# Kernel optimization log

Measured on AMD Instinct MI355X. Metric: run time of the kernel, lower is better.

## Reference

```python
import jax, jax.numpy as jnp
import numpy as np

B = 4096
D = 256
TEMP = 0.5


def setup_inputs() -> dict:
    key = jax.random.key(0)
    k1, k2 = jax.random.split(key)
    x_i = jax.random.normal(k1, (B, D), dtype=jnp.float32)
    x_j = jax.random.normal(k2, (B, D), dtype=jnp.float32)
    return {"x_i": x_i, "x_j": x_j}


def reference(x_i, x_j):
    b = x_i.shape[0]
    # L2-normalize rows (F.normalize with default eps=1e-12)
    def l2norm(x):
        n = jnp.linalg.norm(x, axis=1, keepdims=True)
        return x / jnp.maximum(n, 1e-12)

    z = jnp.concatenate([l2norm(x_i), l2norm(x_j)], axis=0)  # [2B, D]
    # rows of z are unit-norm, so cosine similarity == dot product
    sim = z @ z.T  # [2B, 2B]

    # positives: diagonals at offsets +B and -B
    idx = jnp.arange(b)
    sim_ij = sim[idx, idx + b]
    sim_ji = sim[idx + b, idx]
    pos = jnp.concatenate([sim_ij, sim_ji], axis=0)  # [2B]

    nom = jnp.exp(pos / TEMP)
    neg_mask = 1.0 - jnp.eye(2 * b, dtype=sim.dtype)
    denom = jnp.sum(neg_mask * jnp.exp(sim / TEMP), axis=1)  # [2B]
    loss = jnp.sum(-jnp.log(nom / denom)) / (2 * b)
    return loss
```

## Files before the change

kernel.cpp:

```cpp
#include <hip/hip_runtime.h>

#define NB   4096
#define ND   256
#define N2B  8192
#define INV_T 2.0f
#define NBAND 64
#define NTRI  2080

typedef __attribute__((ext_vector_type(8))) short bf16x8;
typedef __attribute__((ext_vector_type(4))) float f32x4;

__device__ __forceinline__ void gload_lds16(const void* g, void* l) {
  __builtin_amdgcn_global_load_lds(
      (const __attribute__((address_space(1))) void*)g,
      (__attribute__((address_space(3))) void*)l, 16, 0, 0);
}

__device__ __forceinline__ unsigned short f2b(float f) {
  unsigned int u = __float_as_uint(f);
  u = (u + 0x7fffu + ((u >> 16) & 1u)) >> 16;
  return (unsigned short)u;
}
__device__ __forceinline__ float b2f(unsigned short h) {
  return __uint_as_float(((unsigned int)h) << 16);
}

__global__ __launch_bounds__(256) void k_normalize(
    const float* __restrict__ xi, const float* __restrict__ xj,
    unsigned short* __restrict__ Z, float* __restrict__ diagE,
    float* __restrict__ pos, float* __restrict__ lossAcc,
    unsigned int* __restrict__ ticket) {
  __shared__ float sh[2][256];
  if (blockIdx.x == 0 && threadIdx.x == 0) { *lossAcc = 0.0f; *ticket = 0u; }
  int wave = threadIdx.x >> 6, lane = threadIdx.x & 63;
  int r = (int)blockIdx.x * 2 + (wave & 1);
  bool isJ = wave >= 2;
  const float* src = (isJ ? xj : xi) + (size_t)r * ND;
  int zrow = r + (isJ ? NB : 0);

  float4 v = *(const float4*)(src + lane * 4);
  float ss = v.x * v.x + v.y * v.y + v.z * v.z + v.w * v.w;
#pragma unroll
  for (int m = 1; m < 64; m <<= 1) ss += __shfl_xor(ss, m, 64);
  float scale = 1.0f / fmaxf(sqrtf(ss), 1e-12f);
  unsigned short h0 = f2b(v.x * scale), h1 = f2b(v.y * scale);
  unsigned short h2 = f2b(v.z * scale), h3 = f2b(v.w * scale);
  ushort4 st; st.x = h0; st.y = h1; st.z = h2; st.w = h3;
  *(ushort4*)(Z + (size_t)zrow * ND + lane * 4) = st;

  float f0 = b2f(h0), f1 = b2f(h1), f2 = b2f(h2), f3 = b2f(h3);
  float d = f0 * f0 + f1 * f1 + f2 * f2 + f3 * f3;
#pragma unroll
  for (int m = 1; m < 64; m <<= 1) d += __shfl_xor(d, m, 64);
  if (lane == 0) diagE[zrow] = __expf(d * INV_T);

  if (isJ) {
    float* s = sh[wave & 1] + lane * 4;
    s[0] = f0; s[1] = f1; s[2] = f2; s[3] = f3;
  }
  __syncthreads();
  if (!isJ) {
    const float* s = sh[wave] + lane * 4;
    float p = f0 * s[0] + f1 * s[1] + f2 * s[2] + f3 * s[3];
#pragma unroll
    for (int m = 1; m < 64; m <<= 1) p += __shfl_xor(p, m, 64);
    if (lane == 0) pos[r] = p;
  }
}

__global__ __launch_bounds__(512, 4) void k_sym(
    const unsigned short* __restrict__ Z, float* __restrict__ P) {
  __shared__ alignas(16) unsigned short Bs[128 * ND];

  int tid = threadIdx.x;
  int wave = tid >> 6, lane = tid & 63;
  int quad = lane >> 4, c16 = lane & 15;

  int g = ((int)blockIdx.x & 7) * (NTRI / 8) + ((int)blockIdx.x >> 3);
  int SI = 0, SJ = 0, u = g;
  bool found = false;
  for (int si = 0; si < 8 && !found; ++si) {
    for (int sj = si; sj < 8; ++sj) {
      int sz = (si == sj) ? 36 : 64;
      if (u < sz) { SI = si; SJ = sj; found = true; break; }
      u -= sz;
    }
  }
  int ti, tj;
  if (SI == SJ) {
    ti = 0;
    while (u >= 8 - ti) { u -= 8 - ti; ++ti; }
    tj = ti + u;
  } else {
    ti = u >> 3; tj = u & 7;
  }
  int I = SI * 8 + ti, J = SJ * 8 + tj;
  bool diag = (I == J);

  int rowA = I * 128, rowB = J * 128;

  int lr1 = lane >> 5, cs = lane & 31;
#pragma unroll
  for (int j = 0; j < 8; ++j) {
    int r0 = wave * 16 + j * 2;
    int row = r0 + lr1;
    int gc = cs ^ (row & 31);
    gload_lds16(Z + (size_t)(rowB + row) * ND + gc * 8, &Bs[r0 * ND]);
  }

  bf16x8 afr[8];
  int wrow = rowA + wave * 16;
#pragma unroll
  for (int kk = 0; kk < 8; ++kk)
    afr[kk] = *(const bf16x8*)(Z + (size_t)(wrow + c16) * ND + kk * 32 +
                               quad * 8);

  asm volatile("s_waitcnt vmcnt(0)" ::: "memory");
  __syncthreads();

  f32x4 acc[8] = {};
  __builtin_amdgcn_s_setprio(1);
#pragma unroll
  for (int kk = 0; kk < 8; ++kk) {
    bf16x8 bfr[8];
#pragma unroll
    for (int ni = 0; ni < 8; ++ni) {
      int row = ni * 16 + c16;
      int slot = (kk * 4 + quad) ^ (row & 31);
      bfr[ni] = *(const bf16x8*)&Bs[row * ND + slot * 8];
    }
#pragma unroll
    for (int ni = 0; ni < 8; ++ni)
      acc[ni] = __builtin_amdgcn_mfma_f32_16x16x32_bf16(afr[kk], bfr[ni],
                                                        acc[ni], 0, 0, 0);
  }
  __builtin_amdgcn_s_setprio(0);

  float rs[4] = {0.0f, 0.0f, 0.0f, 0.0f};
  float csum[8];
#pragma unroll
  for (int ni = 0; ni < 8; ++ni) csum[ni] = 0.0f;

#pragma unroll
  for (int ni = 0; ni < 8; ++ni)
#pragma unroll
    for (int r = 0; r < 4; ++r) {
      float e = __expf(acc[ni][r] * INV_T);
      rs[r] += e;
      csum[ni] += e;
    }

#pragma unroll
  for (int m = 1; m <= 8; m <<= 1)
#pragma unroll
    for (int r = 0; r < 4; ++r) rs[r] += __shfl_xor(rs[r], m, 64);

#pragma unroll
  for (int r = 0; r < 4; ++r)
    if (c16 == r) {
      int row = wrow + quad * 4 + r;
      P[(size_t)row * NBAND + J] = rs[r];
    }

  if (!diag) {
#pragma unroll
    for (int ni = 0; ni < 8; ++ni) {
      csum[ni] += __shfl_xor(csum[ni], 16, 64);
      csum[ni] += __shfl_xor(csum[ni], 32, 64);
    }
    __syncthreads();
    float* colred = (float*)Bs;
    if (lane < 16) {
#pragma unroll
      for (int ni = 0; ni < 8; ++ni)
        colred[wave * 128 + ni * 16 + lane] = csum[ni];
    }
    __syncthreads();
    if (tid < 128) {
      float v = 0.0f;
#pragma unroll
      for (int w = 0; w < 8; ++w) v += colred[w * 128 + tid];
      P[(size_t)(rowB + tid) * NBAND + I] = v;
    }
  }
}

__global__ __launch_bounds__(256) void k_final(
    const float* __restrict__ P, const float* __restrict__ diagE,
    const float* __restrict__ pos, float* __restrict__ lossAcc,
    unsigned int* __restrict__ ticket, float* __restrict__ out) {
  __shared__ float red[4];
  int tid = threadIdx.x;
  int wave = tid >> 6, lane = tid & 63;
  int row = (int)blockIdx.x * 256 + tid;

  const float4* Pr = (const float4*)(P + (size_t)row * NBAND);
  float s = 0.0f;
#pragma unroll
  for (int q = 0; q < 16; ++q) {
    float4 a = Pr[q];
    s += (a.x + a.y) + (a.z + a.w);
  }
  s -= diagE[row];
  float term = __logf(s) - INV_T * pos[row & (NB - 1)];
#pragma unroll
  for (int m = 1; m < 64; m <<= 1) term += __shfl_xor(term, m, 64);
  if (lane == 0) red[wave] = term;
  __syncthreads();
  if (tid == 0) {
    float bs = red[0] + red[1] + red[2] + red[3];
    atomicAdd(lossAcc, bs);
    __threadfence();
    unsigned int old = atomicAdd(ticket, 1u);
    if (old == 31u) {
      float v = atomicAdd(lossAcc, 0.0f);
      out[0] = v * (1.0f / (float)N2B);
    }
  }
}

extern "C" void kernel_launch(void* const* d_in, const int* in_sizes, int n_in,
                              void* d_out, int out_size, void* d_ws,
                              size_t ws_size, hipStream_t stream) {
  const float* xi = (const float*)d_in[0];
  const float* xj = (const float*)d_in[1];
  float* out = (float*)d_out;
  char* ws = (char*)d_ws;
  unsigned short* Z = (unsigned short*)ws;
  float* P = (float*)(ws + (4u << 20));
  float* pos = (float*)(ws + (6u << 20));
  float* diagE = (float*)(ws + (6u << 20) + 65536);
  float* lossAcc = (float*)(ws + (6u << 20) + 131072);
  unsigned int* ticket = (unsigned int*)(ws + (6u << 20) + 131072 + 64);

  k_normalize<<<dim3(NB / 2), dim3(256), 0, stream>>>(xi, xj, Z, diagE, pos,
                                                      lossAcc, ticket);
  k_sym<<<dim3(NTRI), dim3(512), 0, stream>>>(Z, P);
  k_final<<<dim3(32), dim3(256), 0, stream>>>(P, diagE, pos, lossAcc, ticket,
                                              out);
}
```

Measured before the change: 109.0 us.

## Make k_sym persistent over row strips with double-buffered LDS tiles

Each block now keeps one 128-row A strip resident in registers and walks up to four 128-column B blocks in 64-row half tiles. The next half tile is prefetched into a second LDS buffer while the current one runs through MFMA, and the launch shrinks from 2080 triangular tiles to 544 blocks. The goal is to amortise A loads and block launch and index-decode cost, and to overlap global-to-LDS transfers with compute. In exchange each block has more serial iterations with a barrier per step, fewer blocks are in flight, and some blocks do less work than others, which can leave compute units idle.

```diff
diff --git a/kernel.cpp b/kernel.cpp
--- a/kernel.cpp
+++ b/kernel.cpp
@@ -5,7 +5,7 @@
 #define N2B  8192
 #define INV_T 2.0f
 #define NBAND 64
-#define NTRI  2080
+#define NBLK  544
 
 typedef __attribute__((ext_vector_type(8))) short bf16x8;
 typedef __attribute__((ext_vector_type(4))) float f32x4;
@@ -70,117 +70,128 @@
 
 __global__ __launch_bounds__(512, 4) void k_sym(
     const unsigned short* __restrict__ Z, float* __restrict__ P) {
-  __shared__ alignas(16) unsigned short Bs[128 * ND];
+  __shared__ alignas(16) unsigned short ldsU[32768];
+  __shared__ float colred[2][8][64];
 
   int tid = threadIdx.x;
   int wave = tid >> 6, lane = tid & 63;
   int quad = lane >> 4, c16 = lane & 15;
-
-  int g = ((int)blockIdx.x & 7) * (NTRI / 8) + ((int)blockIdx.x >> 3);
-  int SI = 0, SJ = 0, u = g;
-  bool found = false;
-  for (int si = 0; si < 8 && !found; ++si) {
-    for (int sj = si; sj < 8; ++sj) {
-      int sz = (si == sj) ? 36 : 64;
-      if (u < sz) { SI = si; SJ = sj; found = true; break; }
-      u -= sz;
-    }
-  }
-  int ti, tj;
-  if (SI == SJ) {
-    ti = 0;
-    while (u >= 8 - ti) { u -= 8 - ti; ++ti; }
-    tj = ti + u;
-  } else {
-    ti = u >> 3; tj = u & 7;
-  }
-  int I = SI * 8 + ti, J = SJ * 8 + tj;
-  bool diag = (I == J);
-
-  int rowA = I * 128, rowB = J * 128;
-
   int lr1 = lane >> 5, cs = lane & 31;
+
+  int g = ((int)blockIdx.x & 7) * (NBLK / 8) + ((int)blockIdx.x >> 3);
+  int I = 0, acc0 = 0;
+  while (acc0 + ((64 - I + 3) >> 2) <= g) { acc0 += (64 - I + 3) >> 2; ++I; }
+  int k = g - acc0;
+  int b0 = I + 4 * k;
+  int nb = min(4, 64 - b0);
+  int nt = nb * 2;
+  int q0 = b0 * 2;
+  int rowA = I * 128;
+
 #pragma unroll
   for (int j = 0; j < 8; ++j) {
     int r0 = wave * 16 + j * 2;
     int row = r0 + lr1;
     int gc = cs ^ (row & 31);
-    gload_lds16(Z + (size_t)(rowB + row) * ND + gc * 8, &Bs[r0 * ND]);
-  }
+    gload_lds16(Z + (size_t)(rowA + row) * ND + gc * 8, &ldsU[r0 * ND]);
+  }
+  asm volatile("s_waitcnt vmcnt(0)" ::: "memory");
+  __syncthreads();
 
   bf16x8 afr[8];
+  {
+    int arow = wave * 16 + c16;
+    const unsigned short* ap = &ldsU[arow * ND];
+    int ax = arow & 31;
+#pragma unroll
+    for (int kk = 0; kk < 8; ++kk)
+      afr[kk] = *(const bf16x8*)&ap[((kk * 4 + quad) ^ ax) * 8];
+  }
+  asm volatile("s_waitcnt lgkmcnt(0)" ::: "memory");
+  __syncthreads();
+
+  auto STAGE = [&](int t, int h) {
+    int base = (q0 + t) * 64;
+#pragma unroll
+    for (int j = 0; j < 4; ++j) {
+      int r0 = wave * 8 + j * 2;
+      int row = r0 + lr1;
+      int gc = cs ^ (row & 31);
+      gload_lds16(Z + (size_t)(base + row) * ND + gc * 8,
+                  &ldsU[h * 16384 + r0 * ND]);
+    }
+  };
+
+  STAGE(0, 0);
+  asm volatile("s_waitcnt vmcnt(0)" ::: "memory");
+  __syncthreads();
+
   int wrow = rowA + wave * 16;
-#pragma unroll
-  for (int kk = 0; kk < 8; ++kk)
-    afr[kk] = *(const bf16x8*)(Z + (size_t)(wrow + c16) * ND + kk * 32 +
-                               quad * 8);
-
-  asm volatile("s_waitcnt vmcnt(0)" ::: "memory");
-  __syncthreads();
-
-  f32x4 acc[8] = {};
-  __builtin_amdgcn_s_setprio(1);
-#pragma unroll
-  for (int kk = 0; kk < 8; ++kk) {
-    bf16x8 bfr[8];
-#pragma unroll
-    for (int ni = 0; ni < 8; ++ni) {
-      int row = ni * 16 + c16;
-      int slot = (kk * 4 + quad) ^ (row & 31);
-      bfr[ni] = *(const bf16x8*)&Bs[row * ND + slot * 8];
-    }
-#pragma unroll
-    for (int ni = 0; ni < 8; ++ni)
-      acc[ni] = __builtin_amdgcn_mfma_f32_16x16x32_bf16(afr[kk], bfr[ni],
-                                                        acc[ni], 0, 0, 0);
-  }
-  __builtin_amdgcn_s_setprio(0);
-
   float rs[4] = {0.0f, 0.0f, 0.0f, 0.0f};
-  float csum[8];
-#pragma unroll
-  for (int ni = 0; ni < 8; ++ni) csum[ni] = 0.0f;
-
-#pragma unroll
-  for (int ni = 0; ni < 8; ++ni)
-#pragma unroll
-    for (int r = 0; r < 4; ++r) {
-      float e = __expf(acc[ni][r] * INV_T);
-      rs[r] += e;
-      csum[ni] += e;
-    }
-
-#pragma unroll
-  for (int m = 1; m <= 8; m <<= 1)
-#pragma unroll
-    for (int r = 0; r < 4; ++r) rs[r] += __shfl_xor(rs[r], m, 64);
-
-#pragma unroll
-  for (int r = 0; r < 4; ++r)
-    if (c16 == r) {
-      int row = wrow + quad * 4 + r;
-      P[(size_t)row * NBAND + J] = rs[r];
-    }
-
-  if (!diag) {
-#pragma unroll
-    for (int ni = 0; ni < 8; ++ni) {
-      csum[ni] += __shfl_xor(csum[ni], 16, 64);
-      csum[ni] += __shfl_xor(csum[ni], 32, 64);
-    }
+
+  for (int t = 0; t < nt; ++t) {
+    int h = t & 1;
+    if (t + 1 < nt) STAGE(t + 1, h ^ 1);
+
+    f32x4 acc[4] = {};
+    __builtin_amdgcn_s_setprio(1);
+#pragma unroll
+    for (int kk = 0; kk < 8; ++kk) {
+      bf16x8 bfr[4];
+#pragma unroll
+      for (int ni = 0; ni < 4; ++ni) {
+        int row = ni * 16 + c16;
+        int slot = (kk * 4 + quad) ^ (row & 31);
+        bfr[ni] = *(const bf16x8*)&ldsU[h * 16384 + row * ND + slot * 8];
+      }
+#pragma unroll
+      for (int ni = 0; ni < 4; ++ni)
+        acc[ni] = __builtin_amdgcn_mfma_f32_16x16x32_bf16(afr[kk], bfr[ni],
+                                                          acc[ni], 0, 0, 0);
+    }
+    __builtin_amdgcn_s_setprio(0);
+
+    float cs_[4] = {0.0f, 0.0f, 0.0f, 0.0f};
+#pragma unroll
+    for (int ni = 0; ni < 4; ++ni)
+#pragma unroll
+      for (int r = 0; r < 4; ++r) {
+        float e = __expf(acc[ni][r] * INV_T);
+        rs[r] += e;
+        cs_[ni] += e;
+      }
+#pragma unroll
+    for (int ni = 0; ni < 4; ++ni) {
+      cs_[ni] += __shfl_xor(cs_[ni], 16, 64);
+      cs_[ni] += __shfl_xor(cs_[ni], 32, 64);
+    }
+    if (lane < 16) {
+#pragma unroll
+      for (int ni = 0; ni < 4; ++ni)
+        colred[h][wave][ni * 16 + lane] = cs_[ni];
+    }
+
+    asm volatile("s_waitcnt vmcnt(0)" ::: "memory");
     __syncthreads();
-    float* colred = (float*)Bs;
-    if (lane < 16) {
-#pragma unroll
-      for (int ni = 0; ni < 8; ++ni)
-        colred[wave * 128 + ni * 16 + lane] = csum[ni];
-    }
-    __syncthreads();
-    if (tid < 128) {
+
+    int Jt = b0 + (t >> 1);
+    if (Jt != I && tid < 64) {
       float v = 0.0f;
 #pragma unroll
-      for (int w = 0; w < 8; ++w) v += colred[w * 128 + tid];
-      P[(size_t)(rowB + tid) * NBAND + I] = v;
+      for (int w = 0; w < 8; ++w) v += colred[h][w][tid];
+      P[(size_t)((q0 + t) * 64 + tid) * NBAND + I] = v;
+    }
+    if (t & 1) {
+      float r4[4] = {rs[0], rs[1], rs[2], rs[3]};
+#pragma unroll
+      for (int m = 1; m <= 8; m <<= 1)
+#pragma unroll
+        for (int r = 0; r < 4; ++r) r4[r] += __shfl_xor(r4[r], m, 64);
+#pragma unroll
+      for (int r = 0; r < 4; ++r)
+        if (c16 == r)
+          P[(size_t)(wrow + quad * 4 + r) * NBAND + Jt] = r4[r];
+      rs[0] = rs[1] = rs[2] = rs[3] = 0.0f;
     }
   }
 }
@@ -235,7 +246,7 @@
 
   k_normalize<<<dim3(NB / 2), dim3(256), 0, stream>>>(xi, xj, Z, diagE, pos,
                                                       lossAcc, ticket);
-  k_sym<<<dim3(NTRI), dim3(512), 0, stream>>>(Z, P);
+  k_sym<<<dim3(NBLK), dim3(512), 0, stream>>>(Z, P);
   k_final<<<dim3(32), dim3(256), 0, stream>>>(P, diagE, pos, lossAcc, ticket,
                                               out);
 }
```

Measured after the change: 104.5 us. 4.1% less time.
